# Optimization experiments

Hardware: AMD Instinct MI355X
Metric: run time of the kernel (lower is better)

The kernel has to match this reference:

```python
import jax, jax.numpy as jnp
import numpy as np

N = 8192
F = 64
OUT = 64


def setup_inputs() -> dict:
    key = jax.random.key(0)
    k1, k2, k3 = jax.random.split(key, 3)
    adj = jax.random.uniform(k1, (N, N), dtype=jnp.float32)
    features = jax.random.normal(k2, (N, F), dtype=jnp.float32)
    # torch Linear weight: [out_features, in_features*2], xavier_uniform with relu gain
    gain = float(np.sqrt(2.0))
    fan_in, fan_out = 2 * F, OUT
    bound = gain * float(np.sqrt(6.0 / (fan_in + fan_out)))
    W = jax.random.uniform(k3, (OUT, 2 * F), dtype=jnp.float32, minval=-bound, maxval=bound)
    return {"adj": adj, "features": features, "W": W}


def reference(adj, features, W):
    # neigh = (adj @ x) / (rowsum(adj) + 1)   -- dense 2D branch of SageConvLayer
    deg = jnp.sum(adj, axis=1, keepdims=True) + 1.0          # [N, 1]
    neigh = jnp.matmul(adj, features) / deg                   # [N, F]
    data = jnp.concatenate([features, neigh], axis=-1)        # [N, 2F]
    return jnp.matmul(data, W.T)                              # [N, OUT]
```

## Files before the change

kernel.cpp:

```cpp
#include <hip/hip_runtime.h>

#define NN 8192
#define FF 64
#define NOUT 64

typedef __bf16 bf16x8 __attribute__((ext_vector_type(8)));
typedef float f32x4 __attribute__((ext_vector_type(4)));

__device__ inline bf16x8 cvt8(float4 a, float4 b) {
    bf16x8 r;
    r[0] = (__bf16)a.x; r[1] = (__bf16)a.y; r[2] = (__bf16)a.z; r[3] = (__bf16)a.w;
    r[4] = (__bf16)b.x; r[5] = (__bf16)b.y; r[6] = (__bf16)b.z; r[7] = (__bf16)b.w;
    return r;
}

__global__ void transpose_kernel(const float* __restrict__ feat, __bf16* __restrict__ featT) {
    int g = blockIdx.x * 256 + threadIdx.x;
    int n = g >> 13;
    int k = g & (NN - 1);
    featT[g] = (__bf16)feat[(size_t)k * FF + n];
}

__global__ __launch_bounds__(256, 4)
void main_kernel(const float* __restrict__ adj, const __bf16* __restrict__ featT,
                 __bf16* __restrict__ partN, float* __restrict__ partDeg,
                 int ksMask, int ksShift, int kchunk) {
    int tid = threadIdx.x;
    int w = tid >> 6, lane = tid & 63, ln = lane & 15, q = lane >> 4;
    int ks = blockIdx.x & ksMask;
    int mt = blockIdx.x >> ksShift;
    int rowA = mt * 64 + w * 16 + ln;

    const float*  ap = adj   + (size_t)rowA * NN + ks * kchunk + q * 8;
    const __bf16* bp = featT + (size_t)ln * NN   + ks * kchunk + q * 8;

    f32x4 acc0 = 0, acc1 = 0, acc2 = 0, acc3 = 0, accd = 0;

    bf16x8 ones;
    __bf16 o = (ln == 0) ? (__bf16)1.0f : (__bf16)0.0f;
    #pragma unroll
    for (int i = 0; i < 8; ++i) ones[i] = o;

    int iters = kchunk >> 5;
    #pragma unroll 2
    for (int it = 0; it < iters; ++it) {
        float4 a0 = *(const float4*)ap;
        float4 a1 = *(const float4*)(ap + 4);
        bf16x8 b0 = *(const bf16x8*)(bp);
        bf16x8 b1 = *(const bf16x8*)(bp + 16 * NN);
        bf16x8 b2 = *(const bf16x8*)(bp + 32 * NN);
        bf16x8 b3 = *(const bf16x8*)(bp + 48 * NN);
        bf16x8 af = cvt8(a0, a1);
        acc0 = __builtin_amdgcn_mfma_f32_16x16x32_bf16(af, b0, acc0, 0, 0, 0);
        acc1 = __builtin_amdgcn_mfma_f32_16x16x32_bf16(af, b1, acc1, 0, 0, 0);
        acc2 = __builtin_amdgcn_mfma_f32_16x16x32_bf16(af, b2, acc2, 0, 0, 0);
        acc3 = __builtin_amdgcn_mfma_f32_16x16x32_bf16(af, b3, acc3, 0, 0, 0);
        accd = __builtin_amdgcn_mfma_f32_16x16x32_bf16(af, ones, accd, 0, 0, 0);
        ap += 32;
        bp += 32;
    }

    int growBase = mt * 64 + w * 16 + q * 4;
    #pragma unroll
    for (int r = 0; r < 4; ++r) {
        size_t base = ((size_t)ks * NN + growBase + r) * FF + ln;
        partN[base +  0] = (__bf16)acc0[r];
        partN[base + 16] = (__bf16)acc1[r];
        partN[base + 32] = (__bf16)acc2[r];
        partN[base + 48] = (__bf16)acc3[r];
    }
    if (ln == 0) {
        #pragma unroll
        for (int r = 0; r < 4; ++r)
            partDeg[(size_t)ks * NN + growBase + r] = accd[r];
    }
}

__global__ __launch_bounds__(256)
void epilogue_kernel(const float* __restrict__ feat, const float* __restrict__ W,
                     const __bf16* __restrict__ partN, const float* __restrict__ partDeg,
                     float* __restrict__ out, int KS) {
    __shared__ __bf16 dataB[64][136];
    __shared__ float rdeg[64];
    int tid = threadIdx.x, blk = blockIdx.x;

    if (tid < 64) {
        float s = 0.f;
        for (int ks = 0; ks < KS; ++ks) s += partDeg[(size_t)ks * NN + blk * 64 + tid];
        rdeg[tid] = 1.0f / (s + 1.0f);
    }
    __syncthreads();

    #pragma unroll
    for (int i = 0; i < 16; ++i) {
        int idx = tid + i * 256;
        int r = idx >> 6, c = idx & 63;
        dataB[r][c] = (__bf16)feat[(size_t)(blk * 64 + r) * FF + c];
        float s = 0.f;
        for (int ks = 0; ks < KS; ++ks)
            s += (float)partN[((size_t)ks * NN + blk * 64 + r) * FF + c];
        dataB[r][64 + c] = (__bf16)(s * rdeg[r]);
    }
    __syncthreads();

    int w = tid >> 6, lane = tid & 63, ln = lane & 15, q = lane >> 4;
    f32x4 acc[4];
    #pragma unroll
    for (int t = 0; t < 4; ++t) acc[t] = 0;

    #pragma unroll
    for (int kk = 0; kk < 4; ++kk) {
        bf16x8 af = *(const bf16x8*)&dataB[w * 16 + ln][kk * 32 + q * 8];
        #pragma unroll
        for (int t = 0; t < 4; ++t) {
            const float* wp = W + (size_t)(t * 16 + ln) * 128 + kk * 32 + q * 8;
            float4 b0 = *(const float4*)wp;
            float4 b1 = *(const float4*)(wp + 4);
            bf16x8 bf = cvt8(b0, b1);
            acc[t] = __builtin_amdgcn_mfma_f32_16x16x32_bf16(af, bf, acc[t], 0, 0, 0);
        }
    }

    int grow = blk * 64 + w * 16 + q * 4;
    #pragma unroll
    for (int t = 0; t < 4; ++t)
        #pragma unroll
        for (int r = 0; r < 4; ++r)
            out[(size_t)(grow + r) * NOUT + t * 16 + ln] = acc[t][r];
}

extern "C" void kernel_launch(void* const* d_in, const int* in_sizes, int n_in,
                              void* d_out, int out_size, void* d_ws, size_t ws_size,
                              hipStream_t stream) {
    const float* adj  = (const float*)d_in[0];
    const float* feat = (const float*)d_in[1];
    const float* W    = (const float*)d_in[2];
    float* out = (float*)d_out;
    char* ws = (char*)d_ws;

    int KS = 8, shift = 3;
    while (KS > 1) {
        size_t need = (size_t)(1 << 20) + (size_t)KS * NN * FF * 2 + (size_t)KS * NN * 4;
        if (need <= ws_size) break;
        KS >>= 1; shift--;
    }

    __bf16* featT  = (__bf16*)ws;
    __bf16* partN  = (__bf16*)(ws + (1 << 20));
    float*  partDeg = (float*)(ws + (1 << 20) + (size_t)KS * NN * FF * 2);

    transpose_kernel<<<(NN * FF) / 256, 256, 0, stream>>>(feat, featT);
    main_kernel<<<(NN / 64) * KS, 256, 0, stream>>>(adj, featT, partN, partDeg,
                                                    KS - 1, shift, NN / KS);
    epilogue_kernel<<<NN / 64, 256, 0, stream>>>(feat, W, partN, partDeg, out, KS);
}
```

Before: 445.6 us.

## Double row tile per warp, fix split-K at 16, vectorize transpose and epilogue

Each warp now computes 32 rows of adj times features instead of 16, so every featT B-fragment load feeds two MFMAs. The split-K count is fixed at 16 and the workspace-size fallback is removed. The transpose kernel becomes an LDS-tiled version with vectorized stores, and the epilogue reduces partials with 8-wide bf16 vector loads. The main cost is the adj stream, which is memory bound, so the gain comes mostly from fewer B loads and better side kernels. The risks are higher register pressure and a workspace overflow if ws_size is too small for 16 partial buffers.

```diff
diff --git a/kernel.cpp b/kernel.cpp
--- a/kernel.cpp
+++ b/kernel.cpp
@@ -3,6 +3,8 @@
 #define NN 8192
 #define FF 64
 #define NOUT 64
+#define KS 16
+#define KCHUNK (NN / KS)
 
 typedef __bf16 bf16x8 __attribute__((ext_vector_type(8)));
 typedef float f32x4 __attribute__((ext_vector_type(4)));
@@ -14,92 +16,143 @@
     return r;
 }
 
-__global__ void transpose_kernel(const float* __restrict__ feat, __bf16* __restrict__ featT) {
-    int g = blockIdx.x * 256 + threadIdx.x;
-    int n = g >> 13;
-    int k = g & (NN - 1);
-    featT[g] = (__bf16)feat[(size_t)k * FF + n];
+__global__ __launch_bounds__(256)
+void transpose_kernel(const float* __restrict__ feat, __bf16* __restrict__ featT) {
+    __shared__ __bf16 t[64][72];
+    int tid = threadIdx.x, blk = blockIdx.x;
+    int r = tid >> 2, c0 = (tid & 3) * 16;
+    const float* p = feat + (size_t)(blk * 64 + r) * FF + c0;
+    float4 v0 = *(const float4*)(p);
+    float4 v1 = *(const float4*)(p + 4);
+    float4 v2 = *(const float4*)(p + 8);
+    float4 v3 = *(const float4*)(p + 12);
+    #pragma unroll
+    for (int j = 0; j < 4; ++j) {
+        t[c0 + 0 + j][r]  = (__bf16)(&v0.x)[j];
+        t[c0 + 4 + j][r]  = (__bf16)(&v1.x)[j];
+        t[c0 + 8 + j][r]  = (__bf16)(&v2.x)[j];
+        t[c0 + 12 + j][r] = (__bf16)(&v3.x)[j];
+    }
+    __syncthreads();
+    int n = tid >> 2, co = (tid & 3) * 16;
+    __bf16* dst = featT + (size_t)n * NN + blk * 64 + co;
+    *(bf16x8*)dst       = *(const bf16x8*)&t[n][co];
+    *(bf16x8*)(dst + 8) = *(const bf16x8*)&t[n][co + 8];
 }
 
 __global__ __launch_bounds__(256, 4)
 void main_kernel(const float* __restrict__ adj, const __bf16* __restrict__ featT,
-                 __bf16* __restrict__ partN, float* __restrict__ partDeg,
-                 int ksMask, int ksShift, int kchunk) {
+                 __bf16* __restrict__ partN, float* __restrict__ partDeg) {
     int tid = threadIdx.x;
     int w = tid >> 6, lane = tid & 63, ln = lane & 15, q = lane >> 4;
-    int ks = blockIdx.x & ksMask;
-    int mt = blockIdx.x >> ksShift;
-    int rowA = mt * 64 + w * 16 + ln;
-
-    const float*  ap = adj   + (size_t)rowA * NN + ks * kchunk + q * 8;
-    const __bf16* bp = featT + (size_t)ln * NN   + ks * kchunk + q * 8;
-
-    f32x4 acc0 = 0, acc1 = 0, acc2 = 0, acc3 = 0, accd = 0;
+    int ks = blockIdx.x & (KS - 1);
+    int mt = blockIdx.x >> 4;
+
+    int rowA = mt * 128 + w * 32 + ln;
+    const float*  ap0 = adj + (size_t)rowA * NN + ks * KCHUNK + q * 8;
+    const float*  ap1 = ap0 + (size_t)16 * NN;
+    const __bf16* bp  = featT + (size_t)ln * NN + ks * KCHUNK + q * 8;
+
+    f32x4 acc[2][4], accd[2];
+    #pragma unroll
+    for (int f = 0; f < 2; ++f) {
+        accd[f] = 0;
+        #pragma unroll
+        for (int t = 0; t < 4; ++t) acc[f][t] = 0;
+    }
 
     bf16x8 ones;
     __bf16 o = (ln == 0) ? (__bf16)1.0f : (__bf16)0.0f;
     #pragma unroll
     for (int i = 0; i < 8; ++i) ones[i] = o;
 
-    int iters = kchunk >> 5;
     #pragma unroll 2
-    for (int it = 0; it < iters; ++it) {
-        float4 a0 = *(const float4*)ap;
-        float4 a1 = *(const float4*)(ap + 4);
+    for (int it = 0; it < KCHUNK / 32; ++it) {
+        float4 a0 = *(const float4*)ap0;
+        float4 a1 = *(const float4*)(ap0 + 4);
+        float4 a2 = *(const float4*)ap1;
+        float4 a3 = *(const float4*)(ap1 + 4);
         bf16x8 b0 = *(const bf16x8*)(bp);
         bf16x8 b1 = *(const bf16x8*)(bp + 16 * NN);
         bf16x8 b2 = *(const bf16x8*)(bp + 32 * NN);
         bf16x8 b3 = *(const bf16x8*)(bp + 48 * NN);
-        bf16x8 af = cvt8(a0, a1);
-        acc0 = __builtin_amdgcn_mfma_f32_16x16x32_bf16(af, b0, acc0, 0, 0, 0);
-        acc1 = __builtin_amdgcn_mfma_f32_16x16x32_bf16(af, b1, acc1, 0, 0, 0);
-        acc2 = __builtin_amdgcn_mfma_f32_16x16x32_bf16(af, b2, acc2, 0, 0, 0);
-        acc3 = __builtin_amdgcn_mfma_f32_16x16x32_bf16(af, b3, acc3, 0, 0, 0);
-        accd = __builtin_amdgcn_mfma_f32_16x16x32_bf16(af, ones, accd, 0, 0, 0);
-        ap += 32;
-        bp += 32;
-    }
-
-    int growBase = mt * 64 + w * 16 + q * 4;
-    #pragma unroll
-    for (int r = 0; r < 4; ++r) {
-        size_t base = ((size_t)ks * NN + growBase + r) * FF + ln;
-        partN[base +  0] = (__bf16)acc0[r];
-        partN[base + 16] = (__bf16)acc1[r];
-        partN[base + 32] = (__bf16)acc2[r];
-        partN[base + 48] = (__bf16)acc3[r];
-    }
-    if (ln == 0) {
-        #pragma unroll
-        for (int r = 0; r < 4; ++r)
-            partDeg[(size_t)ks * NN + growBase + r] = accd[r];
+        bf16x8 af0 = cvt8(a0, a1);
+        bf16x8 af1 = cvt8(a2, a3);
+        acc[0][0] = __builtin_amdgcn_mfma_f32_16x16x32_bf16(af0, b0, acc[0][0], 0, 0, 0);
+        acc[1][0] = __builtin_amdgcn_mfma_f32_16x16x32_bf16(af1, b0, acc[1][0], 0, 0, 0);
+        acc[0][1] = __builtin_amdgcn_mfma_f32_16x16x32_bf16(af0, b1, acc[0][1], 0, 0, 0);
+        acc[1][1] = __builtin_amdgcn_mfma_f32_16x16x32_bf16(af1, b1, acc[1][1], 0, 0, 0);
+        acc[0][2] = __builtin_amdgcn_mfma_f32_16x16x32_bf16(af0, b2, acc[0][2], 0, 0, 0);
+        acc[1][2] = __builtin_amdgcn_mfma_f32_16x16x32_bf16(af1, b2, acc[1][2], 0, 0, 0);
+        acc[0][3] = __builtin_amdgcn_mfma_f32_16x16x32_bf16(af0, b3, acc[0][3], 0, 0, 0);
+        acc[1][3] = __builtin_amdgcn_mfma_f32_16x16x32_bf16(af1, b3, acc[1][3], 0, 0, 0);
+        accd[0] = __builtin_amdgcn_mfma_f32_16x16x32_bf16(af0, ones, accd[0], 0, 0, 0);
+        accd[1] = __builtin_amdgcn_mfma_f32_16x16x32_bf16(af1, ones, accd[1], 0, 0, 0);
+        ap0 += 32; ap1 += 32; bp += 32;
+    }
+
+    #pragma unroll
+    for (int f = 0; f < 2; ++f) {
+        int grow = mt * 128 + w * 32 + f * 16 + q * 4;
+        #pragma unroll
+        for (int r = 0; r < 4; ++r) {
+            size_t base = ((size_t)(ks << 13) + grow + r) * FF + ln;
+            partN[base +  0] = (__bf16)acc[f][0][r];
+            partN[base + 16] = (__bf16)acc[f][1][r];
+            partN[base + 32] = (__bf16)acc[f][2][r];
+            partN[base + 48] = (__bf16)acc[f][3][r];
+        }
+        if (ln == 0) {
+            #pragma unroll
+            for (int r = 0; r < 4; ++r)
+                partDeg[(ks << 13) + grow + r] = accd[f][r];
+        }
     }
 }
 
 __global__ __launch_bounds__(256)
 void epilogue_kernel(const float* __restrict__ feat, const float* __restrict__ W,
                      const __bf16* __restrict__ partN, const float* __restrict__ partDeg,
-                     float* __restrict__ out, int KS) {
+                     float* __restrict__ out) {
     __shared__ __bf16 dataB[64][136];
     __shared__ float rdeg[64];
     int tid = threadIdx.x, blk = blockIdx.x;
 
     if (tid < 64) {
         float s = 0.f;
-        for (int ks = 0; ks < KS; ++ks) s += partDeg[(size_t)ks * NN + blk * 64 + tid];
+        #pragma unroll
+        for (int ks = 0; ks < KS; ++ks) s += partDeg[(ks << 13) + blk * 64 + tid];
         rdeg[tid] = 1.0f / (s + 1.0f);
     }
     __syncthreads();
 
     #pragma unroll
-    for (int i = 0; i < 16; ++i) {
+    for (int i = 0; i < 2; ++i) {
         int idx = tid + i * 256;
-        int r = idx >> 6, c = idx & 63;
-        dataB[r][c] = (__bf16)feat[(size_t)(blk * 64 + r) * FF + c];
-        float s = 0.f;
-        for (int ks = 0; ks < KS; ++ks)
-            s += (float)partN[((size_t)ks * NN + blk * 64 + r) * FF + c];
-        dataB[r][64 + c] = (__bf16)(s * rdeg[r]);
+        int r = idx >> 3, c = (idx & 7) * 8;
+        float s[8];
+        #pragma unroll
+        for (int j = 0; j < 8; ++j) s[j] = 0.f;
+        #pragma unroll
+        for (int ks = 0; ks < KS; ++ks) {
+            bf16x8 v = *(const bf16x8*)&partN[((size_t)(ks << 13) + blk * 64 + r) * FF + c];
+            #pragma unroll
+            for (int j = 0; j < 8; ++j) s[j] += (float)v[j];
+        }
+        float rd = rdeg[r];
+        bf16x8 o;
+        #pragma unroll
+        for (int j = 0; j < 8; ++j) o[j] = (__bf16)(s[j] * rd);
+        *(bf16x8*)&dataB[r][64 + c] = o;
+    }
+    #pragma unroll
+    for (int i = 0; i < 2; ++i) {
+        int idx = tid + i * 256;
+        int r = idx >> 3, c = (idx & 7) * 8;
+        const float* p = feat + (size_t)(blk * 64 + r) * FF + c;
+        float4 f0 = *(const float4*)p;
+        float4 f1 = *(const float4*)(p + 4);
+        *(bf16x8*)&dataB[r][c] = cvt8(f0, f1);
     }
     __syncthreads();
 
@@ -138,19 +191,11 @@
     float* out = (float*)d_out;
     char* ws = (char*)d_ws;
 
-    int KS = 8, shift = 3;
-    while (KS > 1) {
-        size_t need = (size_t)(1 << 20) + (size_t)KS * NN * FF * 2 + (size_t)KS * NN * 4;
-        if (need <= ws_size) break;
-        KS >>= 1; shift--;
-    }
-
-    __bf16* featT  = (__bf16*)ws;
-    __bf16* partN  = (__bf16*)(ws + (1 << 20));
+    __bf16* featT   = (__bf16*)ws;
+    __bf16* partN   = (__bf16*)(ws + (1 << 20));
     float*  partDeg = (float*)(ws + (1 << 20) + (size_t)KS * NN * FF * 2);
 
-    transpose_kernel<<<(NN * FF) / 256, 256, 0, stream>>>(feat, featT);
-    main_kernel<<<(NN / 64) * KS, 256, 0, stream>>>(adj, featT, partN, partDeg,
-                                                    KS - 1, shift, NN / KS);
-    epilogue_kernel<<<NN / 64, 256, 0, stream>>>(feat, W, partN, partDeg, out, KS);
-}
+    transpose_kernel<<<NN / 64, 256, 0, stream>>>(feat, featT);
+    main_kernel<<<(NN / 128) * KS, 256, 0, stream>>>(adj, featT, partN, partDeg);
+    epilogue_kernel<<<NN / 64, 256, 0, stream>>>(feat, W, partN, partDeg, out);
+}
```

Result: faster. 381.0 us (-14.5%).
